# Kernel optimization log

Measured on AMD Instinct MI355X. Metric: run time of the kernel, lower is better.

## Reference

```python
import jax, jax.numpy as jnp
import numpy as np

N = 50000      # nodes
IN = 128       # in_channels
H = 2          # heads
C = 64         # hidden_channels (per head)
E = 800000     # edges (before self-loops)
OUT = 40       # out_channels
BN_EPS = 1e-5
NEG_SLOPE = 0.2  # PyG GATConv default


def _bn(x, g, b):
    # BatchNorm1d forward with batch statistics (training-mode math, biased var)
    mu = jnp.mean(x, axis=0)
    v = jnp.var(x, axis=0)
    return (x - mu) * jax.lax.rsqrt(v + BN_EPS) * g + b


def _gat_conv(x, src, dst, W, a_src, a_dst, bias, concat):
    n = x.shape[0]
    h = (x @ W).reshape(n, H, C)                      # [N,H,C] per-head projection
    al_s = jnp.einsum('nhc,hc->nh', h, a_src)         # [N,H]
    al_d = jnp.einsum('nhc,hc->nh', h, a_dst)
    e = jax.nn.leaky_relu(al_s[src] + al_d[dst], NEG_SLOPE)  # [E,H]
    # segment softmax over edges sharing the same destination
    m = jax.ops.segment_max(e, dst, num_segments=n)
    ex = jnp.exp(e - m[dst])
    s = jax.ops.segment_sum(ex, dst, num_segments=n)
    alpha = ex / s[dst]                               # [E,H]
    out = jax.ops.segment_sum(h[src] * alpha[..., None], dst, num_segments=n)  # [N,H,C]
    out = out.reshape(n, H * C) if concat else out.mean(axis=1)
    return out + bias


def setup_inputs() -> dict:
    key = jax.random.key(0)
    ks = jax.random.split(key, 16)
    g = lambda k, shp, scale=1.0: jax.random.normal(k, shp, dtype=jnp.float32) * scale
    x = g(ks[0], (N, IN))
    edge_index = jax.random.randint(ks[1], (2, E), 0, N, dtype=jnp.int32)
    s = 1.0 / np.sqrt(IN)
    s2 = 1.0 / np.sqrt(H * C)
    return {
        'x': x,
        'edge_index': edge_index,
        'bn0_g': jnp.ones((IN,), jnp.float32), 'bn0_b': jnp.zeros((IN,), jnp.float32),
        'W1': g(ks[2], (IN, H * C), s), 'a1_src': g(ks[3], (H, C), s), 'a1_dst': g(ks[4], (H, C), s),
        'b1': jnp.zeros((H * C,), jnp.float32),
        'bn1_g': jnp.ones((H * C,), jnp.float32), 'bn1_b': jnp.zeros((H * C,), jnp.float32),
        'W2': g(ks[5], (H * C, H * C), s2), 'a2_src': g(ks[6], (H, C), s2), 'a2_dst': g(ks[7], (H, C), s2),
        'b2': jnp.zeros((C,), jnp.float32),
        'bn2_g': jnp.ones((C,), jnp.float32), 'bn2_b': jnp.zeros((C,), jnp.float32),
        'Wf': g(ks[8], (C, OUT), 1.0 / np.sqrt(C)), 'bf': jnp.zeros((OUT,), jnp.float32),
    }


def reference(x, edge_index, bn0_g, bn0_b, W1, a1_src, a1_dst, b1, bn1_g, bn1_b,
              W2, a2_src, a2_dst, b2, bn2_g, bn2_b, Wf, bf):
    n = x.shape[0]
    loop = jnp.arange(n, dtype=edge_index.dtype)
    src = jnp.concatenate([edge_index[0], loop])  # add self-loops (PyG default)
    dst = jnp.concatenate([edge_index[1], loop])
    h = _bn(x, bn0_g, bn0_b)
    # layer 1: concat heads
    h = _gat_conv(h, src, dst, W1, a1_src, a1_dst, b1, concat=True)
    h = jax.nn.elu(_bn(h, bn1_g, bn1_b))
    # (dropout is identity in eval mode)
    # layer 2: average heads
    h = _gat_conv(h, src, dst, W2, a2_src, a2_dst, b2, concat=False)
    h = jax.nn.elu(_bn(h, bn2_g, bn2_b))
    return h @ Wf + bf
```

## Files before the change

kernel.cpp:

```cpp
#include <hip/hip_runtime.h>


#define NEG_SLOPE 0.2f
#define BN_EPS 1e-5f

typedef short bf16x8 __attribute__((ext_vector_type(8)));
typedef float f32x4 __attribute__((ext_vector_type(4)));

static __device__ __forceinline__ unsigned short f2bf(float f) {
    union { float f; unsigned u; } v; v.f = f;
    unsigned r = v.u + 0x7FFF + ((v.u >> 16) & 1);
    return (unsigned short)(r >> 16);
}
static __device__ __forceinline__ float2 bf2x2(unsigned v) {
    union { unsigned u; float f; } a, b;
    a.u = v << 16; b.u = v & 0xffff0000u;
    return make_float2(a.f, b.f);
}

__global__ void k_rank(const int* __restrict__ ei, int E, int Nn,
                       int* __restrict__ cnt, int* __restrict__ rank) {
    int i = blockIdx.x * blockDim.x + threadIdx.x;
    if (i >= E + Nn) return;
    int d = (i < E) ? ei[E + i] : (i - E);
    rank[i] = atomicAdd(&cnt[d], 1);
}

__global__ __launch_bounds__(1024) void k_part(const int* __restrict__ cnt, int Nn,
                                               int* __restrict__ part) {
    __shared__ int ws[16];
    int t = threadIdx.x, lane = t & 63, w = t >> 6;
    int i = blockIdx.x * 1024 + t;
    int v = (i < Nn) ? cnt[i] : 0;
    #pragma unroll
    for (int off = 32; off; off >>= 1) v += __shfl_xor(v, off);
    if (lane == 0) ws[w] = v;
    __syncthreads();
    if (t < 16) {
        int s = ws[t];
        #pragma unroll
        for (int off = 8; off; off >>= 1) s += __shfl_xor(s, off);
        if (t == 0) part[blockIdx.x] = s;
    }
}

__global__ __launch_bounds__(64) void k_scanp(int* __restrict__ part, int nb,
                                              int Nn, int* __restrict__ rowptr) {
    int lane = threadIdx.x;
    int carry = 0;
    for (int base = 0; base < nb; base += 64) {
        int i = base + lane;
        int v = (i < nb) ? part[i] : 0;
        int x = v;
        #pragma unroll
        for (int off = 1; off < 64; off <<= 1) {
            int y = __shfl_up(x, off);
            if (lane >= off) x += y;
        }
        if (i < nb) part[i] = carry + x - v;
        carry += __shfl(x, 63);
    }
    if (lane == 0) rowptr[Nn] = carry;
}

__global__ __launch_bounds__(1024) void k_scan2(const int* __restrict__ cnt, int Nn,
                                                const int* __restrict__ part,
                                                int* __restrict__ rowptr) {
    __shared__ int wsum[16];
    int t = threadIdx.x, lane = t & 63, w = t >> 6;
    int i = blockIdx.x * 1024 + t;
    int v = (i < Nn) ? cnt[i] : 0;
    int x = v;
    #pragma unroll
    for (int off = 1; off < 64; off <<= 1) {
        int y = __shfl_up(x, off);
        if (lane >= off) x += y;
    }
    if (lane == 63) wsum[w] = x;
    __syncthreads();
    if (w == 0) {
        int val = (lane < 16) ? wsum[lane] : 0;
        int xs = val;
        #pragma unroll
        for (int off = 1; off < 16; off <<= 1) {
            int y = __shfl_up(xs, off);
            if (lane >= off) xs += y;
        }
        if (lane < 16) wsum[lane] = xs - val;
    }
    __syncthreads();
    if (i < Nn) rowptr[i] = part[blockIdx.x] + wsum[w] + (x - v);
}

__global__ void k_fill2(const int* __restrict__ ei, const int* __restrict__ rank,
                        const int* __restrict__ rowptr, int E, int Nn,
                        int* __restrict__ ssrc) {
    int i = blockIdx.x * blockDim.x + threadIdx.x;
    if (i >= E + Nn) return;
    int s, d;
    if (i < E) { s = ei[i]; d = ei[E + i]; }
    else       { s = i - E; d = s; }
    ssrc[rowptr[d] + rank[i]] = s;
}

template <int C>
__global__ __launch_bounds__(256) void k_bnstat2(const float* __restrict__ x, int M,
                                                 int rowsPerBlock, float* __restrict__ sums) {
    constexpr int TPR = C / 4;
    constexpr int RS  = 256 / TPR;
    __shared__ float red[4][2 * C];
    const int t = threadIdx.x;
    const int cg = t % TPR, rg = t / TPR, w = t >> 6, lane = t & 63;
    int r0 = blockIdx.x * rowsPerBlock + rg;
    int r1 = min(M, blockIdx.x * rowsPerBlock + rowsPerBlock);
    float4 s = make_float4(0, 0, 0, 0), q = make_float4(0, 0, 0, 0);
    #pragma unroll 4
    for (int r = r0; r < r1; r += RS) {
        float4 v = *(const float4*)&x[(size_t)r * C + cg * 4];
        s.x += v.x; s.y += v.y; s.z += v.z; s.w += v.w;
        q.x += v.x * v.x; q.y += v.y * v.y; q.z += v.z * v.z; q.w += v.w * v.w;
    }
    #pragma unroll
    for (int off = TPR; off < 64; off <<= 1) {
        s.x += __shfl_xor(s.x, off); s.y += __shfl_xor(s.y, off);
        s.z += __shfl_xor(s.z, off); s.w += __shfl_xor(s.w, off);
        q.x += __shfl_xor(q.x, off); q.y += __shfl_xor(q.y, off);
        q.z += __shfl_xor(q.z, off); q.w += __shfl_xor(q.w, off);
    }
    if (lane < TPR) {
        *(float4*)&red[w][cg * 4] = s;
        *(float4*)&red[w][C + cg * 4] = q;
    }
    __syncthreads();
    for (int idx = t; idx < 2 * C; idx += 256) {
        float tot = red[0][idx] + red[1][idx] + red[2][idx] + red[3][idx];
        atomicAdd(&sums[idx], tot);
    }
}

__global__ void k_bnfin(const float* __restrict__ sums, int M, int C,
                        const float* __restrict__ g, const float* __restrict__ b,
                        float* __restrict__ st) {
    int c = threadIdx.x;
    if (c < C) {
        float mu = sums[c] / (float)M;
        float var = sums[C + c] / (float)M - mu * mu;
        float s = g[c] * rsqrtf(var + BN_EPS);
        st[c] = s;
        st[C + c] = b[c] - mu * s;
    }
}

__global__ __launch_bounds__(256) void k_prep(const float* __restrict__ in, const float* __restrict__ st,
                                              int M, int elu, unsigned short* __restrict__ outb) {
    int tid = blockIdx.x * 256 + threadIdx.x;
    size_t idx = (size_t)tid * 8;
    if (idx >= (size_t)M * 128) return;
    int ch = (int)(idx & 127);
    float4 v0 = *(const float4*)&in[idx];
    float4 v1 = *(const float4*)&in[idx + 4];
    float4 s0 = *(const float4*)&st[ch];
    float4 s1 = *(const float4*)&st[ch + 4];
    float4 t0 = *(const float4*)&st[128 + ch];
    float4 t1 = *(const float4*)&st[128 + ch + 4];
    float a[8] = {v0.x*s0.x+t0.x, v0.y*s0.y+t0.y, v0.z*s0.z+t0.z, v0.w*s0.w+t0.w,
                  v1.x*s1.x+t1.x, v1.y*s1.y+t1.y, v1.z*s1.z+t1.z, v1.w*s1.w+t1.w};
    if (elu) {
        #pragma unroll
        for (int j = 0; j < 8; j++) a[j] = a[j] > 0.f ? a[j] : expm1f(a[j]);
    }
    uint4 p;
    p.x = ((unsigned)f2bf(a[1]) << 16) | f2bf(a[0]);
    p.y = ((unsigned)f2bf(a[3]) << 16) | f2bf(a[2]);
    p.z = ((unsigned)f2bf(a[5]) << 16) | f2bf(a[4]);
    p.w = ((unsigned)f2bf(a[7]) << 16) | f2bf(a[6]);
    *(uint4*)&outb[idx] = p;
}

__global__ __launch_bounds__(256) void k_wt2(const float* __restrict__ W1, const float* __restrict__ W2,
                                             unsigned short* __restrict__ wt1, unsigned short* __restrict__ wt2) {
    int idx = blockIdx.x * 256 + threadIdx.x;
    if (idx >= 128 * 128) return;
    int n = idx >> 7, k = idx & 127;
    wt1[idx] = f2bf(W1[k * 128 + n]);
    wt2[idx] = f2bf(W2[k * 128 + n]);
}

__global__ __launch_bounds__(256) void k_mfma(
    const unsigned short* __restrict__ abf, const unsigned short* __restrict__ wt,
    const float* __restrict__ asrc, const float* __restrict__ adst, int M,
    unsigned short* __restrict__ hb, float* __restrict__ als, float* __restrict__ ald) {
    __shared__ unsigned short As[64 * 136];
    __shared__ unsigned short Bs[128 * 136];
    const int t = threadIdx.x;
    const int w = t >> 6, lane = t & 63;
    const int c = lane & 15, q = lane >> 4;
    const int row0 = blockIdx.x * 64;

    #pragma unroll
    for (int i = 0; i < 4; i++) {
        int idx = t + i * 256;
        int r = idx >> 4, ch = idx & 15;
        uint4 v = make_uint4(0, 0, 0, 0);
        if (row0 + r < M) v = *(const uint4*)&abf[(size_t)(row0 + r) * 128 + ch * 8];
        *(uint4*)&As[r * 136 + ch * 8] = v;
    }
    #pragma unroll
    for (int i = 0; i < 8; i++) {
        int idx = t + i * 256;
        int r = idx >> 4, ch = idx & 15;
        *(uint4*)&Bs[r * 136 + ch * 8] = *(const uint4*)&wt[(size_t)r * 128 + ch * 8];
    }
    __syncthreads();

    f32x4 acc[8] = {};
    #pragma unroll
    for (int ks = 0; ks < 4; ks++) {
        bf16x8 a = *(bf16x8*)&As[(w * 16 + c) * 136 + (ks * 4 + q) * 8];
        #pragma unroll
        for (int tl = 0; tl < 8; tl++) {
            bf16x8 b = *(bf16x8*)&Bs[(tl * 16 + c) * 136 + (ks * 4 + q) * 8];
            acc[tl] = __builtin_amdgcn_mfma_f32_16x16x32_bf16(a, b, acc[tl], 0, 0, 0);
        }
    }

    #pragma unroll
    for (int reg = 0; reg < 4; reg++) {
        int grow = row0 + w * 16 + q * 4 + reg;
        if (grow < M) {
            #pragma unroll
            for (int tl = 0; tl < 8; tl++)
                hb[(size_t)grow * 128 + tl * 16 + c] = f2bf(acc[tl][reg]);
        }
    }

    float as_[8], ad_[8];
    #pragma unroll
    for (int tl = 0; tl < 8; tl++) { as_[tl] = asrc[tl * 16 + c]; ad_[tl] = adst[tl * 16 + c]; }
    #pragma unroll
    for (int reg = 0; reg < 4; reg++) {
        float s0 = 0.f, s1 = 0.f, d0 = 0.f, d1 = 0.f;
        #pragma unroll
        for (int tl = 0; tl < 4; tl++) { s0 += acc[tl][reg] * as_[tl]; d0 += acc[tl][reg] * ad_[tl]; }
        #pragma unroll
        for (int tl = 4; tl < 8; tl++) { s1 += acc[tl][reg] * as_[tl]; d1 += acc[tl][reg] * ad_[tl]; }
        #pragma unroll
        for (int off = 1; off < 16; off <<= 1) {
            s0 += __shfl_xor(s0, off); s1 += __shfl_xor(s1, off);
            d0 += __shfl_xor(d0, off); d1 += __shfl_xor(d1, off);
        }
        int grow = row0 + w * 16 + q * 4 + reg;
        if (c == 0 && grow < M) {
            *(float2*)&als[(size_t)grow * 2] = make_float2(s0, s1);
            *(float2*)&ald[(size_t)grow * 2] = make_float2(d0, d1);
        }
    }
}

static __device__ __forceinline__ void acc8(float* acc, uint4 v, float a) {
    float2 p;
    p = bf2x2(v.x); acc[0] += a * p.x; acc[1] += a * p.y;
    p = bf2x2(v.y); acc[2] += a * p.x; acc[3] += a * p.y;
    p = bf2x2(v.z); acc[4] += a * p.x; acc[5] += a * p.y;
    p = bf2x2(v.w); acc[6] += a * p.x; acc[7] += a * p.y;
}

template <int MEAN>
static __device__ __forceinline__ void attnagg(
    const int* __restrict__ rowptr, const int* __restrict__ ssrc,
    const float* __restrict__ als, const float* __restrict__ ald,
    float* __restrict__ alpha, const unsigned short* __restrict__ hb,
    const float* __restrict__ bias, int Nn, float* __restrict__ out) {
    int gw = (blockIdx.x * blockDim.x + threadIdx.x) >> 6;
    if (gw >= Nn) return;
    int lane = threadIdx.x & 63;
    int sub = lane >> 4, c = lane & 15, head = c >> 3;
    int beg = rowptr[gw], end = rowptr[gw + 1];
    int deg = end - beg;
    float2 dv = *(const float2*)&ald[(size_t)gw * 2];
    float acc[8] = {};

    if (deg <= 64) {
        bool on = lane < deg;
        int eidx = beg + (on ? lane : 0);
        int sreg = ssrc[eidx];
        float2 av = *(const float2*)&als[(size_t)sreg * 2];
        float v0 = av.x + dv.x; v0 = v0 > 0.f ? v0 : NEG_SLOPE * v0;
        float v1 = av.y + dv.y; v1 = v1 > 0.f ? v1 : NEG_SLOPE * v1;
        float m0 = on ? v0 : -1e30f, m1 = on ? v1 : -1e30f;
        #pragma unroll
        for (int off = 32; off; off >>= 1) {
            m0 = fmaxf(m0, __shfl_xor(m0, off));
            m1 = fmaxf(m1, __shfl_xor(m1, off));
        }
        float p0 = on ? __expf(v0 - m0) : 0.f;
        float p1 = on ? __expf(v1 - m1) : 0.f;
        float t0 = p0, t1 = p1;
        #pragma unroll
        for (int off = 32; off; off >>= 1) {
            t0 += __shfl_xor(t0, off);
            t1 += __shfl_xor(t1, off);
        }
        float al0 = p0 / t0, al1 = p1 / t1;

        int nit = (deg + 3) >> 2;
        for (int it = 0; it < nit; it += 4) {
            #pragma unroll
            for (int u = 0; u < 4; u++) {
                int jj = (it + u) * 4 + sub;
                int ls = jj & 63;
                int sa = __shfl(sreg, ls);
                float a0 = __shfl(al0, ls);
                float a1 = __shfl(al1, ls);
                float aa = head ? a1 : a0;
                if (jj < deg) {
                    uint4 v = *(const uint4*)&hb[(size_t)sa * 128 + c * 8];
                    acc8(acc, v, aa);
                }
            }
        }
    } else {
        float d0 = dv.x, d1 = dv.y;
        float m0 = -1e30f, m1 = -1e30f;
        for (int e = beg + lane; e < end; e += 64) {
            int s = ssrc[e];
            float v0 = als[s * 2] + d0;     v0 = v0 > 0.f ? v0 : NEG_SLOPE * v0;
            float v1 = als[s * 2 + 1] + d1; v1 = v1 > 0.f ? v1 : NEG_SLOPE * v1;
            m0 = fmaxf(m0, v0); m1 = fmaxf(m1, v1);
        }
        #pragma unroll
        for (int off = 32; off; off >>= 1) {
            m0 = fmaxf(m0, __shfl_xor(m0, off));
            m1 = fmaxf(m1, __shfl_xor(m1, off));
        }
        float t0 = 0.f, t1 = 0.f;
        for (int e = beg + lane; e < end; e += 64) {
            int s = ssrc[e];
            float v0 = als[s * 2] + d0;     v0 = v0 > 0.f ? v0 : NEG_SLOPE * v0;
            float v1 = als[s * 2 + 1] + d1; v1 = v1 > 0.f ? v1 : NEG_SLOPE * v1;
            float p0 = __expf(v0 - m0), p1 = __expf(v1 - m1);
            alpha[e * 2] = p0; alpha[e * 2 + 1] = p1;
            t0 += p0; t1 += p1;
        }
        #pragma unroll
        for (int off = 32; off; off >>= 1) {
            t0 += __shfl_xor(t0, off);
            t1 += __shfl_xor(t1, off);
        }
        float i0 = 1.f / t0, i1 = 1.f / t1;
        for (int e = beg + sub; e < end; e += 4) {
            int s = ssrc[e];
            float a = (head ? alpha[(size_t)e * 2 + 1] * i1 : alpha[(size_t)e * 2] * i0);
            uint4 v = *(const uint4*)&hb[(size_t)s * 128 + c * 8];
            acc8(acc, v, a);
        }
    }

    #pragma unroll
    for (int j2 = 0; j2 < 8; j2++) {
        acc[j2] += __shfl_xor(acc[j2], 16);
        acc[j2] += __shfl_xor(acc[j2], 32);
        if (MEAN) acc[j2] += __shfl_xor(acc[j2], 8);
    }
    if (MEAN) {
        if (sub == 0 && c < 8) {
            float4 b0 = *(const float4*)&bias[c * 8];
            float4 b1 = *(const float4*)&bias[c * 8 + 4];
            float4 o0 = make_float4(0.5f * acc[0] + b0.x, 0.5f * acc[1] + b0.y, 0.5f * acc[2] + b0.z, 0.5f * acc[3] + b0.w);
            float4 o1 = make_float4(0.5f * acc[4] + b1.x, 0.5f * acc[5] + b1.y, 0.5f * acc[6] + b1.z, 0.5f * acc[7] + b1.w);
            *(float4*)&out[(size_t)gw * 64 + c * 8] = o0;
            *(float4*)&out[(size_t)gw * 64 + c * 8 + 4] = o1;
        }
    } else {
        if (sub == 0) {
            float4 b0 = *(const float4*)&bias[c * 8];
            float4 b1 = *(const float4*)&bias[c * 8 + 4];
            float4 o0 = make_float4(acc[0] + b0.x, acc[1] + b0.y, acc[2] + b0.z, acc[3] + b0.w);
            float4 o1 = make_float4(acc[4] + b1.x, acc[5] + b1.y, acc[6] + b1.z, acc[7] + b1.w);
            *(float4*)&out[(size_t)gw * 128 + c * 8] = o0;
            *(float4*)&out[(size_t)gw * 128 + c * 8 + 4] = o1;
        }
    }
}

__global__ __launch_bounds__(256) void k_attnagg1(const int* __restrict__ rowptr, const int* __restrict__ ssrc,
                                                  const float* __restrict__ als, const float* __restrict__ ald,
                                                  float* __restrict__ alpha, const unsigned short* __restrict__ hb,
                                                  const float* __restrict__ bias, int Nn, float* __restrict__ out) {
    attnagg<0>(rowptr, ssrc, als, ald, alpha, hb, bias, Nn, out);
}

__global__ __launch_bounds__(256) void k_attnagg2(const int* __restrict__ rowptr, const int* __restrict__ ssrc,
                                                  const float* __restrict__ als, const float* __restrict__ ald,
                                                  float* __restrict__ alpha, const unsigned short* __restrict__ hb,
                                                  const float* __restrict__ bias, int Nn, float* __restrict__ out) {
    attnagg<1>(rowptr, ssrc, als, ald, alpha, hb, bias, Nn, out);
}

__global__ __launch_bounds__(128) void k_gemmf(const float* __restrict__ A, const float* __restrict__ Wf,
                                               const float* __restrict__ bf, const float* __restrict__ st,
                                               int M, float* __restrict__ out) {
    __shared__ float As[128 * 65];
    __shared__ float Bs[64 * 40];
    int t = threadIdx.x;
    int row0 = blockIdx.x * 128;
    for (int i = t; i < 64 * 40; i += 128) Bs[i] = Wf[i];
    for (int i = t; i < 128 * 64; i += 128) {
        int r = i >> 6, k = i & 63;
        int gr = row0 + r;
        float v = 0.f;
        if (gr < M) {
            v = A[(size_t)gr * 64 + k] * st[k] + st[64 + k];
            v = v > 0.f ? v : expm1f(v);
        }
        As[r * 65 + k] = v;
    }
    __syncthreads();
    int cg = t & 3, rg = t >> 2;
    float acc[4][10] = {};
    for (int k = 0; k < 64; k++) {
        float b[10];
        #pragma unroll
        for (int j = 0; j < 10; j++) b[j] = Bs[k * 40 + cg * 10 + j];
        #pragma unroll
        for (int r = 0; r < 4; r++) {
            float a = As[(rg * 4 + r) * 65 + k];
            #pragma unroll
            for (int j = 0; j < 10; j++) acc[r][j] += a * b[j];
        }
    }
    for (int r = 0; r < 4; r++) {
        int gr = row0 + rg * 4 + r;
        if (gr < M) {
            #pragma unroll
            for (int j = 0; j < 10; j++) out[(size_t)gr * 40 + cg * 10 + j] = acc[r][j] + bf[cg * 10 + j];
        }
    }
}

extern "C" void kernel_launch(void* const* d_in, const int* in_sizes, int n_in,
                              void* d_out, int out_size, void* d_ws, size_t ws_size,
                              hipStream_t stream) {
    const float* x     = (const float*)d_in[0];
    const int*   ei    = (const int*)d_in[1];
    const float* bn0_g = (const float*)d_in[2];
    const float* bn0_b = (const float*)d_in[3];
    const float* W1    = (const float*)d_in[4];
    const float* a1s   = (const float*)d_in[5];
    const float* a1d   = (const float*)d_in[6];
    const float* b1    = (const float*)d_in[7];
    const float* bn1_g = (const float*)d_in[8];
    const float* bn1_b = (const float*)d_in[9];
    const float* W2    = (const float*)d_in[10];
    const float* a2s   = (const float*)d_in[11];
    const float* a2d   = (const float*)d_in[12];
    const float* b2    = (const float*)d_in[13];
    const float* bn2_g = (const float*)d_in[14];
    const float* bn2_b = (const float*)d_in[15];
    const float* Wf    = (const float*)d_in[16];
    const float* bf    = (const float*)d_in[17];
    float* out = (float*)d_out;

    const int N  = in_sizes[0] / 128;
    const int E  = in_sizes[1] / 2;
    const int ET = E + N;

    char* ws = (char*)d_ws;
    size_t off = 0;
    auto alloc = [&](size_t bytes) -> char* {
        char* p = ws + off;
        off = (off + bytes + 255) & ~(size_t)255;
        return p;
    };
    int*   cnt    = (int*)alloc((size_t)N * 4);
    int*   rowptr = (int*)alloc((size_t)(N + 1) * 4);
    int*   ssrc   = (int*)alloc((size_t)ET * 4);
    float* abuf   = (float*)alloc((size_t)N * 128 * 4);
    unsigned short* abf = (unsigned short*)alloc((size_t)N * 128 * 2);
    unsigned short* hb  = (unsigned short*)alloc((size_t)N * 128 * 2);
    unsigned short* wt1 = (unsigned short*)alloc((size_t)128 * 128 * 2);
    unsigned short* wt2 = (unsigned short*)alloc((size_t)128 * 128 * 2);
    float* als    = (float*)alloc((size_t)N * 2 * 4);
    float* ald    = (float*)alloc((size_t)N * 2 * 4);
    int*   part   = (int*)alloc(1024 * 4);
    float* sums   = (float*)alloc(640 * 4);
    float* st     = (float*)alloc(256 * 4);
    int*   rank   = (int*)hb;
    float* alpha  = (float*)abf;

    const int tb = 256;
    const int egrid = (ET + tb - 1) / tb;
    const int wgrid = ((size_t)N * 64 + tb - 1) / tb;
    const int pgrid = ((size_t)N * 16 + tb - 1) / tb;
    const int ggrid = (N + 63) / 64;
    const int nscan = (N + 1023) / 1024;
    const int bgrid = (N + 255) / 256;

    hipMemsetAsync(cnt, 0, (size_t)N * 4, stream);
    hipMemsetAsync(sums, 0, 640 * 4, stream);
    k_rank<<<egrid, tb, 0, stream>>>(ei, E, N, cnt, rank);
    k_part<<<nscan, 1024, 0, stream>>>(cnt, N, part);
    k_scanp<<<1, 64, 0, stream>>>(part, nscan, N, rowptr);
    k_scan2<<<nscan, 1024, 0, stream>>>(cnt, N, part, rowptr);
    k_fill2<<<egrid, tb, 0, stream>>>(ei, rank, rowptr, E, N, ssrc);

    k_wt2<<<64, tb, 0, stream>>>(W1, W2, wt1, wt2);

    k_bnstat2<128><<<bgrid, 256, 0, stream>>>(x, N, 256, sums);
    k_bnfin<<<1, 128, 0, stream>>>(sums, N, 128, bn0_g, bn0_b, st);

    k_prep<<<pgrid, tb, 0, stream>>>(x, st, N, 0, abf);
    k_mfma<<<ggrid, tb, 0, stream>>>(abf, wt1, a1s, a1d, N, hb, als, ald);
    k_attnagg1<<<wgrid, tb, 0, stream>>>(rowptr, ssrc, als, ald, alpha, hb, b1, N, abuf);

    k_bnstat2<128><<<bgrid, 256, 0, stream>>>(abuf, N, 256, sums + 256);
    k_bnfin<<<1, 128, 0, stream>>>(sums + 256, N, 128, bn1_g, bn1_b, st);

    k_prep<<<pgrid, tb, 0, stream>>>(abuf, st, N, 1, abf);
    k_mfma<<<ggrid, tb, 0, stream>>>(abf, wt2, a2s, a2d, N, hb, als, ald);
    k_attnagg2<<<wgrid, tb, 0, stream>>>(rowptr, ssrc, als, ald, alpha, hb, b2, N, abuf);

    k_bnstat2<64><<<bgrid, 256, 0, stream>>>(abuf, N, 256, sums + 512);
    k_bnfin<<<1, 64, 0, stream>>>(sums + 512, N, 64, bn2_g, bn2_b, st);

    k_gemmf<<<(N + 127) / 128, 128, 0, stream>>>(abuf, Wf, bf, st, N, out);
}
```

Before: 341.1 us.

## Fuse BN/ELU prep into MFMA tile load and pack attention weights as half2

Removes the separate k_prep kernel and its bf16 intermediate buffer by applying the batchnorm scale/shift and optional ELU while loading fp32 rows into shared memory inside the MFMA GEMM. In the aggregation loop, the two per-head attention coefficients are packed into one half2 register so only one shuffle is needed per edge instead of two, and the loop is restructured to process two edges per iteration. The alpha buffer gets its own allocation now that abf is gone. The GEMM now reads fp32 input (twice the bytes), and alpha drops to fp16 precision.

```diff
diff --git a/kernel.cpp b/kernel.cpp
--- a/kernel.cpp
+++ b/kernel.cpp
@@ -1,4 +1,5 @@
 #include <hip/hip_runtime.h>
+#include <hip/hip_fp16.h>
 
 
 #define NEG_SLOPE 0.2f
@@ -16,6 +17,10 @@
     union { unsigned u; float f; } a, b;
     a.u = v << 16; b.u = v & 0xffff0000u;
     return make_float2(a.f, b.f);
+}
+static __device__ __forceinline__ float halfsel(unsigned p, int head) {
+    __half2 h = *(__half2*)&p;
+    return head ? __high2float(h) : __low2float(h);
 }
 
 __global__ void k_rank(const int* __restrict__ ei, int E, int Nn,
@@ -151,32 +156,6 @@
     }
 }
 
-__global__ __launch_bounds__(256) void k_prep(const float* __restrict__ in, const float* __restrict__ st,
-                                              int M, int elu, unsigned short* __restrict__ outb) {
-    int tid = blockIdx.x * 256 + threadIdx.x;
-    size_t idx = (size_t)tid * 8;
-    if (idx >= (size_t)M * 128) return;
-    int ch = (int)(idx & 127);
-    float4 v0 = *(const float4*)&in[idx];
-    float4 v1 = *(const float4*)&in[idx + 4];
-    float4 s0 = *(const float4*)&st[ch];
-    float4 s1 = *(const float4*)&st[ch + 4];
-    float4 t0 = *(const float4*)&st[128 + ch];
-    float4 t1 = *(const float4*)&st[128 + ch + 4];
-    float a[8] = {v0.x*s0.x+t0.x, v0.y*s0.y+t0.y, v0.z*s0.z+t0.z, v0.w*s0.w+t0.w,
-                  v1.x*s1.x+t1.x, v1.y*s1.y+t1.y, v1.z*s1.z+t1.z, v1.w*s1.w+t1.w};
-    if (elu) {
-        #pragma unroll
-        for (int j = 0; j < 8; j++) a[j] = a[j] > 0.f ? a[j] : expm1f(a[j]);
-    }
-    uint4 p;
-    p.x = ((unsigned)f2bf(a[1]) << 16) | f2bf(a[0]);
-    p.y = ((unsigned)f2bf(a[3]) << 16) | f2bf(a[2]);
-    p.z = ((unsigned)f2bf(a[5]) << 16) | f2bf(a[4]);
-    p.w = ((unsigned)f2bf(a[7]) << 16) | f2bf(a[6]);
-    *(uint4*)&outb[idx] = p;
-}
-
 __global__ __launch_bounds__(256) void k_wt2(const float* __restrict__ W1, const float* __restrict__ W2,
                                              unsigned short* __restrict__ wt1, unsigned short* __restrict__ wt2) {
     int idx = blockIdx.x * 256 + threadIdx.x;
@@ -187,7 +166,8 @@
 }
 
 __global__ __launch_bounds__(256) void k_mfma(
-    const unsigned short* __restrict__ abf, const unsigned short* __restrict__ wt,
+    const float* __restrict__ A, const unsigned short* __restrict__ wt,
+    const float* __restrict__ stp, int elu,
     const float* __restrict__ asrc, const float* __restrict__ adst, int M,
     unsigned short* __restrict__ hb, float* __restrict__ als, float* __restrict__ ald) {
     __shared__ unsigned short As[64 * 136];
@@ -198,12 +178,27 @@
     const int row0 = blockIdx.x * 64;
 
     #pragma unroll
-    for (int i = 0; i < 4; i++) {
+    for (int i = 0; i < 8; i++) {
         int idx = t + i * 256;
-        int r = idx >> 4, ch = idx & 15;
-        uint4 v = make_uint4(0, 0, 0, 0);
-        if (row0 + r < M) v = *(const uint4*)&abf[(size_t)(row0 + r) * 128 + ch * 8];
-        *(uint4*)&As[r * 136 + ch * 8] = v;
+        int r = idx >> 5, ch4 = idx & 31;
+        int gr = row0 + r;
+        float4 v = make_float4(0, 0, 0, 0);
+        if (gr < M) {
+            v = *(const float4*)&A[(size_t)gr * 128 + ch4 * 4];
+            float4 sc = *(const float4*)&stp[ch4 * 4];
+            float4 sh = *(const float4*)&stp[128 + ch4 * 4];
+            v.x = v.x * sc.x + sh.x; v.y = v.y * sc.y + sh.y;
+            v.z = v.z * sc.z + sh.z; v.w = v.w * sc.w + sh.w;
+            if (elu) {
+                v.x = v.x > 0.f ? v.x : expm1f(v.x);
+                v.y = v.y > 0.f ? v.y : expm1f(v.y);
+                v.z = v.z > 0.f ? v.z : expm1f(v.z);
+                v.w = v.w > 0.f ? v.w : expm1f(v.w);
+            }
+        }
+        unsigned p0 = ((unsigned)f2bf(v.y) << 16) | f2bf(v.x);
+        unsigned p1 = ((unsigned)f2bf(v.w) << 16) | f2bf(v.z);
+        *(uint2*)&As[r * 136 + ch4 * 4] = make_uint2(p0, p1);
     }
     #pragma unroll
     for (int i = 0; i < 8; i++) {
@@ -301,22 +296,26 @@
             t0 += __shfl_xor(t0, off);
             t1 += __shfl_xor(t1, off);
         }
-        float al0 = p0 / t0, al1 = p1 / t1;
+        __half2 hpk = __floats2half2_rn(p0 / t0, p1 / t1);
+        int pk = *(int*)&hpk;
 
         int nit = (deg + 3) >> 2;
-        for (int it = 0; it < nit; it += 4) {
-            #pragma unroll
-            for (int u = 0; u < 4; u++) {
-                int jj = (it + u) * 4 + sub;
-                int ls = jj & 63;
-                int sa = __shfl(sreg, ls);
-                float a0 = __shfl(al0, ls);
-                float a1 = __shfl(al1, ls);
-                float aa = head ? a1 : a0;
-                if (jj < deg) {
-                    uint4 v = *(const uint4*)&hb[(size_t)sa * 128 + c * 8];
-                    acc8(acc, v, aa);
-                }
+        for (int it = 0; it < nit; it += 2) {
+            int j0 = it * 4 + sub;
+            int j1 = j0 + 4;
+            int sa = __shfl(sreg, j0 & 63);
+            int sb = __shfl(sreg, j1 & 63);
+            unsigned pa = (unsigned)__shfl(pk, j0 & 63);
+            unsigned pb = (unsigned)__shfl(pk, j1 & 63);
+            float aa = halfsel(pa, head);
+            float ab = halfsel(pb, head);
+            if (j0 < deg) {
+                uint4 va = *(const uint4*)&hb[(size_t)sa * 128 + c * 8];
+                acc8(acc, va, aa);
+            }
+            if (j1 < deg) {
+                uint4 vb = *(const uint4*)&hb[(size_t)sb * 128 + c * 8];
+                acc8(acc, vb, ab);
             }
         }
     } else {
@@ -476,22 +475,20 @@
     int*   rowptr = (int*)alloc((size_t)(N + 1) * 4);
     int*   ssrc   = (int*)alloc((size_t)ET * 4);
     float* abuf   = (float*)alloc((size_t)N * 128 * 4);
-    unsigned short* abf = (unsigned short*)alloc((size_t)N * 128 * 2);
     unsigned short* hb  = (unsigned short*)alloc((size_t)N * 128 * 2);
     unsigned short* wt1 = (unsigned short*)alloc((size_t)128 * 128 * 2);
     unsigned short* wt2 = (unsigned short*)alloc((size_t)128 * 128 * 2);
+    float* alpha  = (float*)alloc((size_t)ET * 2 * 4);
     float* als    = (float*)alloc((size_t)N * 2 * 4);
     float* ald    = (float*)alloc((size_t)N * 2 * 4);
     int*   part   = (int*)alloc(1024 * 4);
     float* sums   = (float*)alloc(640 * 4);
     float* st     = (float*)alloc(256 * 4);
     int*   rank   = (int*)hb;
-    float* alpha  = (float*)abf;
 
     const int tb = 256;
     const int egrid = (ET + tb - 1) / tb;
     const int wgrid = ((size_t)N * 64 + tb - 1) / tb;
-    const int pgrid = ((size_t)N * 16 + tb - 1) / tb;
     const int ggrid = (N + 63) / 64;
     const int nscan = (N + 1023) / 1024;
     const int bgrid = (N + 255) / 256;
@@ -509,15 +506,13 @@
     k_bnstat2<128><<<bgrid, 256, 0, stream>>>(x, N, 256, sums);
     k_bnfin<<<1, 128, 0, stream>>>(sums, N, 128, bn0_g, bn0_b, st);
 
-    k_prep<<<pgrid, tb, 0, stream>>>(x, st, N, 0, abf);
-    k_mfma<<<ggrid, tb, 0, stream>>>(abf, wt1, a1s, a1d, N, hb, als, ald);
+    k_mfma<<<ggrid, tb, 0, stream>>>(x, wt1, st, 0, a1s, a1d, N, hb, als, ald);
     k_attnagg1<<<wgrid, tb, 0, stream>>>(rowptr, ssrc, als, ald, alpha, hb, b1, N, abuf);
 
     k_bnstat2<128><<<bgrid, 256, 0, stream>>>(abuf, N, 256, sums + 256);
     k_bnfin<<<1, 128, 0, stream>>>(sums + 256, N, 128, bn1_g, bn1_b, st);
 
-    k_prep<<<pgrid, tb, 0, stream>>>(abuf, st, N, 1, abf);
-    k_mfma<<<ggrid, tb, 0, stream>>>(abf, wt2, a2s, a2d, N, hb, als, ald);
+    k_mfma<<<ggrid, tb, 0, stream>>>(abuf, wt2, st, 1, a2s, a2d, N, hb, als, ald);
     k_attnagg2<<<wgrid, tb, 0, stream>>>(rowptr, ssrc, als, ald, alpha, hb, b2, N, abuf);
 
     k_bnstat2<64><<<bgrid, 256, 0, stream>>>(abuf, N, 256, sums + 512);
```

After: 340.4 us. Within noise of the previous version (-0.2%).
